# Performance work log

Measured on AMD Instinct MI355X. Metric: run time of the kernel, lower is better.

Reference implementation:

```python
import jax, jax.numpy as jnp
import numpy as np

B, N, H, IN, D, ET = 16, 128, 256, 4, 2, 2
E = N * (N - 1)
NRF = 4 * D + 1            # num_relative_features = 9 (2D)
NODE_F = IN + NRF + D      # 15
EDGE_F = 2 * NRF + IN + D  # 24
EPS = 1e-8


def _norm(v):
    return jnp.sqrt(jnp.sum(v * v, axis=-1, keepdims=True) + EPS)


def _rot(R, v):
    return jnp.einsum('...ij,...j->...i', R, v)


def _relfeat(dp, dv, R, dth):
    # rotation-invariant relative features in frame R: rotated rel pos/vel,
    # distances, polar angles, heading difference -> 2+2+1+1+1+1+1 = 9 dims
    rp = _rot(R, dp)
    rv = _rot(R, dv)
    ang = jnp.arctan2(rp[..., 1:2], rp[..., 0:1])
    vang = jnp.arctan2(rv[..., 1:2], rv[..., 0:1])
    return jnp.concatenate([rp, rv, _norm(dp), ang, _norm(dv), vang, dth], -1)


def _forward(inputs, hidden, edges, predicted_field,
             msg_fc1_w, msg_fc1_b, msg_fc2_w, msg_fc2_b,
             pm_fc1_w, pm_fc1_b, pm_fc2_w, pm_fc2_b,
             hidden_r_w, hidden_i_w, hidden_h_w,
             present_r_w, present_r_b, present_i_w, present_i_b,
             present_n_w, present_n_b,
             input_r_w, input_r_b, input_i_w, input_i_b, input_n_w, input_n_b,
             out_w1, out_b1, out_w2, out_b2, out_w3, out_b3,
             send, recv):
    # ---- recurrent message passing on hidden state ----
    pre_msg = jnp.concatenate([hidden[:, recv], hidden[:, send]], -1)  # [B,E,2H]
    all_msgs = jnp.zeros((B, E, H), pre_msg.dtype)
    for i in range(1, ET):  # skip_first_edge_type = True
        m = jnp.tanh(pre_msg @ msg_fc1_w[i].T + msg_fc1_b[i])
        m = jnp.tanh(m @ msg_fc2_w[i].T + msg_fc2_b[i])
        all_msgs = all_msgs + m * edges[:, :, i:i + 1]
    agg_msgs = jnp.zeros((B, N, H), all_msgs.dtype).at[:, recv].add(all_msgs) / (N - 1)

    # ---- localizer: per-node frame from velocity heading ----
    ext = jnp.concatenate([inputs, predicted_field], -1)  # [B,N,6]
    pos, vel, field = ext[..., :D], ext[..., D:2 * D], ext[..., 2 * D:]
    theta = jnp.arctan2(vel[..., 1], vel[..., 0])  # [B,N]
    c, s = jnp.cos(theta), jnp.sin(theta)
    R = jnp.stack([jnp.stack([c, s], -1), jnp.stack([-s, c], -1)], -2)  # [B,N,2,2]
    Rinv = jnp.swapaxes(R, -1, -2)

    loc_pos, loc_vel, loc_field = _rot(R, pos), _rot(R, vel), _rot(R, field)
    rel_self = _relfeat(pos, vel, R, theta[..., None])
    rel_feat = jnp.concatenate([rel_self, loc_pos, loc_vel, loc_field], -1)  # [B,N,15]

    dp = pos[:, send] - pos[:, recv]
    dv = vel[:, send] - vel[:, recv]
    dth = (theta[:, send] - theta[:, recv])[..., None]
    f1 = _relfeat(dp, dv, R[:, recv], dth)
    f2 = _relfeat(-dp, -dv, R[:, send], -dth)
    edge_attr = jnp.concatenate(
        [f1, f2, loc_pos[:, recv], loc_vel[:, recv], loc_field[:, recv]], -1)  # [B,E,24]

    # ---- present (observation) message passing ----
    present_msgs = jnp.zeros((B, E, H), edge_attr.dtype)
    for i in range(1, ET):
        m = jax.nn.relu(edge_attr @ pm_fc1_w[i].T + pm_fc1_b[i])
        m = jax.nn.relu(m @ pm_fc2_w[i].T + pm_fc2_b[i])
        present_msgs = present_msgs + m * edges[:, :, i:i + 1]
    present_agg = jnp.zeros((B, N, H), present_msgs.dtype).at[:, recv].add(present_msgs) / (N - 1)

    # ---- GRU-style gated update ----
    inp_r = rel_feat @ input_r_w.T + input_r_b + present_agg @ present_r_w.T + present_r_b
    inp_i = rel_feat @ input_i_w.T + input_i_b + present_agg @ present_i_w.T + present_i_b
    inp_n = rel_feat @ input_n_w.T + input_n_b + present_agg @ present_n_w.T + present_n_b
    r = jax.nn.sigmoid(inp_r + agg_msgs @ hidden_r_w.T)
    i_g = jax.nn.sigmoid(inp_i + agg_msgs @ hidden_i_w.T)
    n_g = jnp.tanh(inp_n + r * (agg_msgs @ hidden_h_w.T))
    hidden_new = (1.0 - i_g) * n_g + i_g * hidden

    # ---- output MLP + globalizer ----
    h1 = jax.nn.relu(hidden_new @ out_w1.T + out_b1)
    h2 = jax.nn.relu(h1 @ out_w2.T + out_b2)
    pred = h2 @ out_w3.T + out_b3  # [B,N,4]
    pred_global = jnp.concatenate(
        [_rot(Rinv, pred[..., :D]), _rot(Rinv, pred[..., D:2 * D])], -1)
    outputs = inputs + pred_global
    return outputs, hidden_new


def setup_inputs():
    key = jax.random.key(0)
    ks = iter(jax.random.split(key, 48))
    rn = lambda *s: jax.random.normal(next(ks), s, jnp.float32)
    w = lambda *s: rn(*s) * 0.05
    send, recv = np.where(~np.eye(N, dtype=bool))
    return dict(
        inputs=rn(B, N, IN), hidden=rn(B, N, H),
        edges=jax.random.uniform(next(ks), (B, E, ET), jnp.float32),
        predicted_field=rn(B, N, D),
        msg_fc1_w=w(ET, H, 2 * H), msg_fc1_b=w(ET, H),
        msg_fc2_w=w(ET, H, H), msg_fc2_b=w(ET, H),
        pm_fc1_w=w(ET, H, EDGE_F), pm_fc1_b=w(ET, H),
        pm_fc2_w=w(ET, H, H), pm_fc2_b=w(ET, H),
        hidden_r_w=w(H, H), hidden_i_w=w(H, H), hidden_h_w=w(H, H),
        present_r_w=w(H, H), present_r_b=w(H),
        present_i_w=w(H, H), present_i_b=w(H),
        present_n_w=w(H, H), present_n_b=w(H),
        input_r_w=w(H, NODE_F), input_r_b=w(H),
        input_i_w=w(H, NODE_F), input_i_b=w(H),
        input_n_w=w(H, NODE_F), input_n_b=w(H),
        out_w1=w(H, H), out_b1=w(H), out_w2=w(H, H), out_b2=w(H),
        out_w3=w(IN, H), out_b3=w(IN),
        send_edges=jnp.asarray(send, jnp.int32),
        recv_edges=jnp.asarray(recv, jnp.int32),
    )


def reference(inputs, hidden, edges, predicted_field,
              msg_fc1_w, msg_fc1_b, msg_fc2_w, msg_fc2_b,
              pm_fc1_w, pm_fc1_b, pm_fc2_w, pm_fc2_b,
              hidden_r_w, hidden_i_w, hidden_h_w,
              present_r_w, present_r_b, present_i_w, present_i_b,
              present_n_w, present_n_b,
              input_r_w, input_r_b, input_i_w, input_i_b, input_n_w, input_n_b,
              out_w1, out_b1, out_w2, out_b2, out_w3, out_b3,
              send_edges, recv_edges):
    return _forward(inputs, hidden, edges, predicted_field,
                    msg_fc1_w, msg_fc1_b, msg_fc2_w, msg_fc2_b,
                    pm_fc1_w, pm_fc1_b, pm_fc2_w, pm_fc2_b,
                    hidden_r_w, hidden_i_w, hidden_h_w,
                    present_r_w, present_r_b, present_i_w, present_i_b,
                    present_n_w, present_n_b,
                    input_r_w, input_r_b, input_i_w, input_i_b, input_n_w, input_n_b,
                    out_w1, out_b1, out_w2, out_b2, out_w3, out_b3,
                    send_edges, recv_edges)
```

## Files before the change

kernel.cpp:

```cpp
#include <hip/hip_runtime.h>
#include <math.h>

#define BB 16
#define NN 128
#define HH 256
#define EE (NN*(NN-1))

typedef unsigned short ushort_t;
typedef unsigned int uint_t;
typedef __attribute__((ext_vector_type(8))) short bf16x8;
typedef __attribute__((ext_vector_type(4))) float f32x4;

__device__ __forceinline__ ushort_t f2b(float f) {
  unsigned u = __builtin_bit_cast(unsigned, f);
  unsigned r = (u + 0x7fffu + ((u >> 16) & 1u)) >> 16;
  return (ushort_t)r;
}
__device__ __forceinline__ float blo(uint_t u) {
  return __builtin_bit_cast(float, u << 16);
}
__device__ __forceinline__ float bhi(uint_t u) {
  return __builtin_bit_cast(float, u & 0xffff0000u);
}

__device__ __forceinline__ float fast_tanh(float x) {
  float xx = fminf(fmaxf(x, -15.f), 15.f);
  float e = __builtin_amdgcn_exp2f(xx * 2.8853900817779268f);
  return (e - 1.f) * __builtin_amdgcn_rcpf(e + 1.f);
}
__device__ __forceinline__ float fast_sigmoid(float x) {
  float xx = fminf(fmaxf(x, -30.f), 30.f);
  float e = __builtin_amdgcn_exp2f(-xx * 1.4426950408889634f);
  return __builtin_amdgcn_rcpf(1.f + e);
}

__global__ __launch_bounds__(256) void k_prep(
    const float* __restrict__ inputs, const float* __restrict__ pfield,
    float* __restrict__ geom, float* __restrict__ relf,
    const float* __restrict__ w2, const float* __restrict__ pw2,
    const float* __restrict__ pw1,
    const float* __restrict__ pr_w, const float* __restrict__ pi_w,
    const float* __restrict__ pn_w, const float* __restrict__ hr_w,
    const float* __restrict__ hi_w, const float* __restrict__ hh_w,
    const float* __restrict__ ow1, const float* __restrict__ ow2,
    const float* __restrict__ w1,
    ushort_t* __restrict__ w2b, ushort_t* __restrict__ pw2b,
    ushort_t* __restrict__ pw1b, uint_t* __restrict__ wpk) {
  __shared__ float ltile[64][65];
  int bid = blockIdx.x;
  int tid = threadIdx.x;

  if (bid < 8) {
    int idx = bid * 256 + tid;
    float px = inputs[idx*4+0], py = inputs[idx*4+1];
    float vx = inputs[idx*4+2], vy = inputs[idx*4+3];
    float fx = pfield[idx*2+0], fy = pfield[idx*2+1];
    float th = atan2f(vy, vx);
    float c = cosf(th), s = sinf(th);
    float lpx =  c*px + s*py, lpy = -s*px + c*py;
    float lvx =  c*vx + s*vy, lvy = -s*vx + c*vy;
    float lfx =  c*fx + s*fy, lfy = -s*fx + c*fy;
    float np_ = sqrtf(px*px + py*py + 1e-8f);
    float nv_ = sqrtf(vx*vx + vy*vy + 1e-8f);
    float ang  = atan2f(lpy, lpx);
    float vang = atan2f(lvy, lvx);
    float* g = geom + idx*16;
    g[0]=px; g[1]=py; g[2]=vx; g[3]=vy; g[4]=th; g[5]=c; g[6]=s;
    g[7]=lpx; g[8]=lpy; g[9]=lvx; g[10]=lvy; g[11]=lfx; g[12]=lfy;
    float* r = relf + idx*16;
    r[0]=lpx; r[1]=lpy; r[2]=lvx; r[3]=lvy; r[4]=np_; r[5]=ang; r[6]=nv_; r[7]=vang; r[8]=th;
    r[9]=lpx; r[10]=lpy; r[11]=lvx; r[12]=lvy; r[13]=lfx; r[14]=lfy;
    return;
  }
  if (bid < 552) {
    int idx = (bid - 8) * 256 + tid;
    if (idx < HH*HH) { w2b[idx] = f2b(w2[HH*HH + idx]); return; }
    idx -= HH*HH;
    if (idx < HH*HH) { pw2b[idx] = f2b(pw2[HH*HH + idx]); return; }
    idx -= HH*HH;
    int col = idx >> 5, kk = idx & 31;
    pw1b[idx] = (kk < 24) ? f2b(pw1[col*24 + kk]) : (ushort_t)0;
    return;
  }
  int tb = bid - 552;
  int m  = tb >> 4;
  int sub = tb & 15;
  int Hbase  = (sub >> 2) * 64;
  int k2base = (sub & 3) * 32;
  const float* src; int sstride, soff;
  if      (m == 0) { src = pr_w; sstride = HH; soff = 0; }
  else if (m == 1) { src = pi_w; sstride = HH; soff = 0; }
  else if (m == 2) { src = pn_w; sstride = HH; soff = 0; }
  else if (m == 3) { src = hr_w; sstride = HH; soff = 0; }
  else if (m == 4) { src = hi_w; sstride = HH; soff = 0; }
  else if (m == 5) { src = hh_w; sstride = HH; soff = 0; }
  else if (m == 6) { src = ow1;  sstride = HH; soff = 0; }
  else if (m == 7) { src = ow2;  sstride = HH; soff = 0; }
  else if (m == 8) { src = w1 + HH*2*HH; sstride = 2*HH; soff = 0; }
  else             { src = w1 + HH*2*HH; sstride = 2*HH; soff = HH; }
  int wv = tid >> 6, lane = tid & 63;
  #pragma unroll 4
  for (int i = 0; i < 16; ++i) {
    int rl = wv*16 + i;
    ltile[rl][lane] = src[(Hbase + rl)*sstride + soff + 2*k2base + lane];
  }
  __syncthreads();
  int h_l = tid & 63, kslot = tid >> 6;
  uint_t* dst = wpk + m*32768;
  #pragma unroll
  for (int e = 0; e < 8; ++e) {
    int kk = kslot*8 + e;
    uint_t lo = f2b(ltile[h_l][2*kk]);
    uint_t hi = f2b(ltile[h_l][2*kk + 1]);
    dst[(k2base + kk)*256 + Hbase + h_l] = lo | (hi << 16);
  }
}

__global__ __launch_bounds__(256) void k_hab(const float* __restrict__ hidden,
                                             const uint_t* __restrict__ wpk,
                                             const float* __restrict__ b1,
                                             float* __restrict__ Ha,
                                             float* __restrict__ Hb) {
  int n = blockIdx.x >> 2, qtr = blockIdx.x & 3;
  int tid = threadIdx.x;
  __shared__ float x[4][HH];
  for (int q = 0; q < 4; ++q) {
    int b = qtr*4 + q;
    x[q][tid] = hidden[(b*NN + n)*HH + tid];
  }
  __syncthreads();
  const uint_t* pA = wpk + 8*32768;
  const uint_t* pB = wpk + 9*32768;
  float accA[4], accB[4];
  float bias = b1[HH + tid];
  #pragma unroll
  for (int q = 0; q < 4; ++q) { accA[q] = bias; accB[q] = 0.f; }
  for (int k2 = 0; k2 < 128; ++k2) {
    uint_t ua = pA[(k2<<8) + tid];
    uint_t ub = pB[(k2<<8) + tid];
    float wa0 = blo(ua), wa1 = bhi(ua);
    float wb0 = blo(ub), wb1 = bhi(ub);
    int k = k2 << 1;
    #pragma unroll
    for (int q = 0; q < 4; ++q) {
      float2 x2 = *(const float2*)(&x[q][k]);
      accA[q] += x2.x*wa0 + x2.y*wa1;
      accB[q] += x2.x*wb0 + x2.y*wb1;
    }
  }
  for (int q = 0; q < 4; ++q) {
    int b = qtr*4 + q;
    Ha[(b*NN + n)*HH + tid] = accA[q];
    Hb[(b*NN + n)*HH + tid] = accB[q];
  }
}

__global__ __launch_bounds__(256, 4) void k_edge(
    const float* __restrict__ Ha, const float* __restrict__ Hb,
    const float* __restrict__ geom, const float* __restrict__ edges,
    const ushort_t* __restrict__ w2b, const float* __restrict__ b2,
    const ushort_t* __restrict__ pw2b, const float* __restrict__ pb2,
    const ushort_t* __restrict__ pw1b, const float* __restrict__ pb1,
    float* __restrict__ agg0, float* __restrict__ agg1,
    float* __restrict__ pagg0, float* __restrict__ pagg1) {
  int half = blockIdx.x & 1;
  int j = (blockIdx.x >> 1) & 127;
  int b = blockIdx.x >> 8;
  int tid = threadIdx.x;
  int lane = tid & 63;
  int wv = tid >> 6;
  int lrow = lane & 15, lk = lane >> 4;

  __shared__ __align__(16) unsigned char m1s[64*512];
  __shared__ __align__(16) unsigned char attrB[64*64];
  __shared__ __align__(16) float HajS[HH];
  __shared__ float wgtS[64];
  __shared__ float gjS[13];

  HajS[tid] = Ha[(b*NN + j)*HH + tid];
  if (tid < 13) gjS[tid] = geom[(b*NN + j)*16 + tid];
  __syncthreads();

  if (tid < 64) {
    int il = tid;
    int i = half*64 + il;
    const float* gi = geom + (b*NN + i)*16;
    float dpx = gi[0]-gjS[0], dpy = gi[1]-gjS[1];
    float dvx = gi[2]-gjS[2], dvy = gi[3]-gjS[3];
    float dth = gi[4]-gjS[4];
    float cj = gjS[5], sj = gjS[6];
    float ci = gi[5],  si = gi[6];
    float ndp = sqrtf(dpx*dpx + dpy*dpy + 1e-8f);
    float ndv = sqrtf(dvx*dvx + dvy*dvy + 1e-8f);
    float r1x =  cj*dpx + sj*dpy, r1y = -sj*dpx + cj*dpy;
    float v1x =  cj*dvx + sj*dvy, v1y = -sj*dvx + cj*dvy;
    float r2x = -(ci*dpx + si*dpy), r2y = si*dpx - ci*dpy;
    float v2x = -(ci*dvx + si*dvy), v2y = si*dvx - ci*dvy;
    float f[24];
    f[0]=r1x; f[1]=r1y; f[2]=v1x; f[3]=v1y;
    f[4]=ndp; f[5]=atan2f(r1y, r1x);
    f[6]=ndv; f[7]=atan2f(v1y, v1x); f[8]=dth;
    f[9]=r2x; f[10]=r2y; f[11]=v2x; f[12]=v2y;
    f[13]=ndp; f[14]=atan2f(r2y, r2x);
    f[15]=ndv; f[16]=atan2f(v2y, v2x); f[17]=-dth;
    f[18]=gjS[7]; f[19]=gjS[8]; f[20]=gjS[9];
    f[21]=gjS[10]; f[22]=gjS[11]; f[23]=gjS[12];
    #pragma unroll
    for (int kb = 0; kb < 4; ++kb) {
      bf16x8 v;
      #pragma unroll
      for (int e = 0; e < 8; ++e) {
        int k = kb*8 + e;
        v[e] = (k < 24) ? (short)f2b(f[k]) : (short)0;
      }
      *reinterpret_cast<bf16x8*>(attrB + il*64 + ((kb*16) ^ ((il&3)<<4))) = v;
    }
    float w = 0.f;
    if (i != j) {
      int e = i*127 + (j < i ? j : j-1);
      w = edges[(b*EE + e)*2 + 1];
    }
    wgtS[il] = w;
  }
  __syncthreads();

  {
    int hp = tid & 127;
    int rh = tid >> 7;
    float2 ha2 = *(const float2*)(HajS + 2*hp);
    const float* hbbase = Hb + (b*NN + half*64 + rh*32)*HH + 2*hp;
    #pragma unroll
    for (int r0 = 0; r0 < 32; r0 += 8) {
      float2 v[8];
      #pragma unroll
      for (int u = 0; u < 8; ++u)
        v[u] = *(const float2*)(hbbase + (r0+u)*HH);
      #pragma unroll
      for (int u = 0; u < 8; ++u) {
        int row = rh*32 + r0 + u;
        uint_t lo = f2b(fast_tanh(ha2.x + v[u].x));
        uint_t hi = f2b(fast_tanh(ha2.y + v[u].y));
        *(uint_t*)(m1s + row*512 + ((hp*4) ^ ((row&15)<<4))) = lo | (hi << 16);
      }
    }
  }
  __syncthreads();

  float wreg[16];
  #pragma unroll
  for (int rt = 0; rt < 4; ++rt)
    #pragma unroll
    for (int r = 0; r < 4; ++r)
      wreg[rt*4+r] = wgtS[rt*16 + lk*4 + r];

  {
    f32x4 acc[4][4];
    {
      float bias0 = b2[wv*64 + 0*16 + lrow];
      float bias1 = b2[wv*64 + 1*16 + lrow];
      float bias2 = b2[wv*64 + 2*16 + lrow];
      float bias3 = b2[wv*64 + 3*16 + lrow];
      #pragma unroll
      for (int rt = 0; rt < 4; ++rt) {
        acc[rt][0] = (f32x4){bias0,bias0,bias0,bias0};
        acc[rt][1] = (f32x4){bias1,bias1,bias1,bias1};
        acc[rt][2] = (f32x4){bias2,bias2,bias2,bias2};
        acc[rt][3] = (f32x4){bias3,bias3,bias3,bias3};
      }
    }
    for (int kk = 0; kk < 8; ++kk) {
      bf16x8 afr[4];
      #pragma unroll
      for (int rt = 0; rt < 4; ++rt) {
        int row = rt*16 + lrow;
        afr[rt] = *reinterpret_cast<const bf16x8*>(
            m1s + row*512 + ((kk*64 + lk*16) ^ ((row&15)<<4)));
      }
      #pragma unroll
      for (int nt = 0; nt < 4; ++nt) {
        int col = wv*64 + nt*16 + lrow;
        bf16x8 bfr = *reinterpret_cast<const bf16x8*>(w2b + col*HH + kk*32 + lk*8);
        #pragma unroll
        for (int rt = 0; rt < 4; ++rt)
          acc[rt][nt] = __builtin_amdgcn_mfma_f32_16x16x32_bf16(afr[rt], bfr, acc[rt][nt], 0, 0, 0);
      }
    }
    float* aggOut = half ? agg1 : agg0;
    #pragma unroll
    for (int nt = 0; nt < 4; ++nt) {
      float p = 0.f;
      #pragma unroll
      for (int rt = 0; rt < 4; ++rt)
        #pragma unroll
        for (int r = 0; r < 4; ++r)
          p += fast_tanh(acc[rt][nt][r]) * wreg[rt*4+r];
      p += __shfl_xor(p, 16);
      p += __shfl_xor(p, 32);
      if (lane < 16)
        aggOut[(b*NN + j)*HH + wv*64 + nt*16 + lane] = p * (1.0f/127.0f);
    }
  }
  __syncthreads();

  {
    f32x4 acc[4][4];
    {
      float bias0 = pb1[wv*64 + 0*16 + lrow];
      float bias1 = pb1[wv*64 + 1*16 + lrow];
      float bias2 = pb1[wv*64 + 2*16 + lrow];
      float bias3 = pb1[wv*64 + 3*16 + lrow];
      #pragma unroll
      for (int rt = 0; rt < 4; ++rt) {
        acc[rt][0] = (f32x4){bias0,bias0,bias0,bias0};
        acc[rt][1] = (f32x4){bias1,bias1,bias1,bias1};
        acc[rt][2] = (f32x4){bias2,bias2,bias2,bias2};
        acc[rt][3] = (f32x4){bias3,bias3,bias3,bias3};
      }
    }
    bf16x8 afr[4];
    #pragma unroll
    for (int rt = 0; rt < 4; ++rt) {
      int row = rt*16 + lrow;
      afr[rt] = *reinterpret_cast<const bf16x8*>(
          attrB + row*64 + ((lk*16) ^ ((lrow&3)<<4)));
    }
    #pragma unroll
    for (int nt = 0; nt < 4; ++nt) {
      int col = wv*64 + nt*16 + lrow;
      bf16x8 bfr = *reinterpret_cast<const bf16x8*>(pw1b + col*32 + lk*8);
      #pragma unroll
      for (int rt = 0; rt < 4; ++rt)
        acc[rt][nt] = __builtin_amdgcn_mfma_f32_16x16x32_bf16(afr[rt], bfr, acc[rt][nt], 0, 0, 0);
    }
    #pragma unroll
    for (int nt = 0; nt < 4; ++nt) {
      int col = wv*64 + nt*16 + lrow;
      #pragma unroll
      for (int rt = 0; rt < 4; ++rt)
        #pragma unroll
        for (int r = 0; r < 4; ++r) {
          int row = rt*16 + lk*4 + r;
          *(ushort_t*)(m1s + row*512 + ((col*2) ^ ((row&15)<<4))) =
              f2b(fmaxf(acc[rt][nt][r], 0.f));
        }
    }
  }
  __syncthreads();

  {
    f32x4 acc[4][4];
    {
      float bias0 = pb2[wv*64 + 0*16 + lrow];
      float bias1 = pb2[wv*64 + 1*16 + lrow];
      float bias2 = pb2[wv*64 + 2*16 + lrow];
      float bias3 = pb2[wv*64 + 3*16 + lrow];
      #pragma unroll
      for (int rt = 0; rt < 4; ++rt) {
        acc[rt][0] = (f32x4){bias0,bias0,bias0,bias0};
        acc[rt][1] = (f32x4){bias1,bias1,bias1,bias1};
        acc[rt][2] = (f32x4){bias2,bias2,bias2,bias2};
        acc[rt][3] = (f32x4){bias3,bias3,bias3,bias3};
      }
    }
    for (int kk = 0; kk < 8; ++kk) {
      bf16x8 afr[4];
      #pragma unroll
      for (int rt = 0; rt < 4; ++rt) {
        int row = rt*16 + lrow;
        afr[rt] = *reinterpret_cast<const bf16x8*>(
            m1s + row*512 + ((kk*64 + lk*16) ^ ((row&15)<<4)));
      }
      #pragma unroll
      for (int nt = 0; nt < 4; ++nt) {
        int col = wv*64 + nt*16 + lrow;
        bf16x8 bfr = *reinterpret_cast<const bf16x8*>(pw2b + col*HH + kk*32 + lk*8);
        #pragma unroll
        for (int rt = 0; rt < 4; ++rt)
          acc[rt][nt] = __builtin_amdgcn_mfma_f32_16x16x32_bf16(afr[rt], bfr, acc[rt][nt], 0, 0, 0);
      }
    }
    float* paggOut = half ? pagg1 : pagg0;
    #pragma unroll
    for (int nt = 0; nt < 4; ++nt) {
      float p = 0.f;
      #pragma unroll
      for (int rt = 0; rt < 4; ++rt)
        #pragma unroll
        for (int r = 0; r < 4; ++r)
          p += fmaxf(acc[rt][nt][r], 0.f) * wreg[rt*4+r];
      p += __shfl_xor(p, 16);
      p += __shfl_xor(p, 32);
      if (lane < 16)
        paggOut[(b*NN + j)*HH + wv*64 + nt*16 + lane] = p * (1.0f/127.0f);
    }
  }
}

__global__ __launch_bounds__(256) void k_gru(
    const float* __restrict__ inputs, const float* __restrict__ hidden,
    const float* __restrict__ geom, const float* __restrict__ relf,
    const float* __restrict__ agg0, const float* __restrict__ agg1,
    const float* __restrict__ pagg0, const float* __restrict__ pagg1,
    const uint_t* __restrict__ wpk,
    const float* __restrict__ pr_b, const float* __restrict__ pi_b,
    const float* __restrict__ pn_b,
    const float* __restrict__ ir_w, const float* __restrict__ ir_b,
    const float* __restrict__ ii_w, const float* __restrict__ ii_b,
    const float* __restrict__ in_w, const float* __restrict__ in_b,
    const float* __restrict__ ob1, const float* __restrict__ ob2,
    const float* __restrict__ ow3, const float* __restrict__ ob3,
    float* __restrict__ out_o, float* __restrict__ out_h) {
  int n = blockIdx.x >> 2, qtr = blockIdx.x & 3;
  int tid = threadIdx.x;
  __shared__ float paS[4][HH], agS[4][HH], hS[4][HH], t0S[4][HH], t1S[4][HH];
  __shared__ float relS[4][16];
  __shared__ float predS[4][4];

  for (int q = 0; q < 4; ++q) {
    int b = qtr*4 + q;
    int base = (b*NN + n)*HH;
    paS[q][tid] = pagg0[base + tid] + pagg1[base + tid];
    agS[q][tid] = agg0[base + tid] + agg1[base + tid];
    hS[q][tid]  = hidden[base + tid];
  }
  if (tid < 64) {
    int q = tid >> 4, k = tid & 15;
    int b = qtr*4 + q;
    relS[q][k] = (k < 15) ? relf[(b*NN + n)*16 + k] : 0.f;
  }
  __syncthreads();

  int h = tid;
  const uint_t* pPr = wpk;
  const uint_t* pPi = wpk + 32768;
  const uint_t* pPn = wpk + 2*32768;
  const uint_t* pHr = wpk + 3*32768;
  const uint_t* pHi = wpk + 4*32768;
  const uint_t* pHh = wpk + 5*32768;
  const uint_t* pO1 = wpk + 6*32768;
  const uint_t* pO2 = wpk + 7*32768;

  float aR[4], aI[4], aN[4], aH[4];
  float br = ir_b[h] + pr_b[h];
  float bi = ii_b[h] + pi_b[h];
  float bn = in_b[h] + pn_b[h];
  #pragma unroll
  for (int q = 0; q < 4; ++q) { aR[q]=br; aI[q]=bi; aN[q]=bn; aH[q]=0.f; }

  for (int k = 0; k < 15; ++k) {
    float wr = ir_w[h*15+k], wi = ii_w[h*15+k], wn = in_w[h*15+k];
    #pragma unroll
    for (int q = 0; q < 4; ++q) {
      float x = relS[q][k];
      aR[q] += x*wr; aI[q] += x*wi; aN[q] += x*wn;
    }
  }

  for (int k2 = 0; k2 < 128; ++k2) {
    uint_t upr = pPr[(k2<<8) + h];
    uint_t upi = pPi[(k2<<8) + h];
    uint_t upn = pPn[(k2<<8) + h];
    uint_t uhr = pHr[(k2<<8) + h];
    uint_t uhi = pHi[(k2<<8) + h];
    uint_t uhh = pHh[(k2<<8) + h];
    float pr0 = blo(upr), pr1 = bhi(upr);
    float pi0 = blo(upi), pi1 = bhi(upi);
    float pn0 = blo(upn), pn1 = bhi(upn);
    float hr0 = blo(uhr), hr1 = bhi(uhr);
    float hi0 = blo(uhi), hi1 = bhi(uhi);
    float hh0 = blo(uhh), hh1 = bhi(uhh);
    int k = k2 << 1;
    #pragma unroll
    for (int q = 0; q < 4; ++q) {
      float2 xp = *(const float2*)(&paS[q][k]);
      float2 xa = *(const float2*)(&agS[q][k]);
      aR[q] += xp.x*pr0 + xp.y*pr1 + xa.x*hr0 + xa.y*hr1;
      aI[q] += xp.x*pi0 + xp.y*pi1 + xa.x*hi0 + xa.y*hi1;
      aN[q] += xp.x*pn0 + xp.y*pn1;
      aH[q] += xa.x*hh0 + xa.y*hh1;
    }
  }

  #pragma unroll
  for (int q = 0; q < 4; ++q) {
    int b = qtr*4 + q;
    float r  = fast_sigmoid(aR[q]);
    float ig = fast_sigmoid(aI[q]);
    float ng = fast_tanh(aN[q] + r*aH[q]);
    float hn = (1.f - ig)*ng + ig*hS[q][h];
    out_h[(b*NN + n)*HH + h] = hn;
    t0S[q][h] = hn;
  }
  __syncthreads();

  {
    float a1[4];
    float bias = ob1[h];
    #pragma unroll
    for (int q = 0; q < 4; ++q) a1[q] = bias;
    for (int k2 = 0; k2 < 128; ++k2) {
      uint_t u = pO1[(k2<<8) + h];
      float w0 = blo(u), w1 = bhi(u);
      int k = k2 << 1;
      #pragma unroll
      for (int q = 0; q < 4; ++q) {
        float2 x2 = *(const float2*)(&t0S[q][k]);
        a1[q] += x2.x*w0 + x2.y*w1;
      }
    }
    __syncthreads();
    #pragma unroll
    for (int q = 0; q < 4; ++q) t1S[q][h] = fmaxf(a1[q], 0.f);
  }
  __syncthreads();

  {
    float a2[4];
    float bias = ob2[h];
    #pragma unroll
    for (int q = 0; q < 4; ++q) a2[q] = bias;
    for (int k2 = 0; k2 < 128; ++k2) {
      uint_t u = pO2[(k2<<8) + h];
      float w0 = blo(u), w1 = bhi(u);
      int k = k2 << 1;
      #pragma unroll
      for (int q = 0; q < 4; ++q) {
        float2 x2 = *(const float2*)(&t1S[q][k]);
        a2[q] += x2.x*w0 + x2.y*w1;
      }
    }
    __syncthreads();
    #pragma unroll
    for (int q = 0; q < 4; ++q) t0S[q][h] = fmaxf(a2[q], 0.f);
  }
  __syncthreads();

  if (tid < 16) {
    int o = tid >> 2, q = tid & 3;
    float acc = ob3[o];
    for (int k = 0; k < HH; ++k) acc += t0S[q][k]*ow3[o*HH + k];
    predS[q][o] = acc;
  }
  __syncthreads();
  if (tid < 4) {
    int q = tid;
    int b = qtr*4 + q;
    const float* g = geom + (b*NN + n)*16;
    float c = g[5], s = g[6];
    float p0 = predS[q][0], p1 = predS[q][1], p2 = predS[q][2], p3 = predS[q][3];
    int base = (b*NN + n)*4;
    out_o[base+0] = inputs[base+0] + (c*p0 - s*p1);
    out_o[base+1] = inputs[base+1] + (s*p0 + c*p1);
    out_o[base+2] = inputs[base+2] + (c*p2 - s*p3);
    out_o[base+3] = inputs[base+3] + (s*p2 + c*p3);
  }
}

extern "C" void kernel_launch(void* const* d_in, const int* in_sizes, int n_in,
                              void* d_out, int out_size, void* d_ws, size_t ws_size,
                              hipStream_t stream) {
  const float* inputs    = (const float*)d_in[0];
  const float* hidden    = (const float*)d_in[1];
  const float* edges     = (const float*)d_in[2];
  const float* pfield    = (const float*)d_in[3];
  const float* msg_fc1_w = (const float*)d_in[4];
  const float* msg_fc1_b = (const float*)d_in[5];
  const float* msg_fc2_w = (const float*)d_in[6];
  const float* msg_fc2_b = (const float*)d_in[7];
  const float* pm_fc1_w  = (const float*)d_in[8];
  const float* pm_fc1_b  = (const float*)d_in[9];
  const float* pm_fc2_w  = (const float*)d_in[10];
  const float* pm_fc2_b  = (const float*)d_in[11];
  const float* hr_w = (const float*)d_in[12];
  const float* hi_w = (const float*)d_in[13];
  const float* hh_w = (const float*)d_in[14];
  const float* pr_w = (const float*)d_in[15];
  const float* pr_b = (const float*)d_in[16];
  const float* pi_w = (const float*)d_in[17];
  const float* pi_b = (const float*)d_in[18];
  const float* pn_w = (const float*)d_in[19];
  const float* pn_b = (const float*)d_in[20];
  const float* ir_w = (const float*)d_in[21];
  const float* ir_b = (const float*)d_in[22];
  const float* ii_w = (const float*)d_in[23];
  const float* ii_b = (const float*)d_in[24];
  const float* in_w = (const float*)d_in[25];
  const float* in_b = (const float*)d_in[26];
  const float* ow1  = (const float*)d_in[27];
  const float* ob1  = (const float*)d_in[28];
  const float* ow2  = (const float*)d_in[29];
  const float* ob2  = (const float*)d_in[30];
  const float* ow3  = (const float*)d_in[31];
  const float* ob3  = (const float*)d_in[32];

  float* ws   = (float*)d_ws;
  float* geom = ws;
  float* relf = geom + 32768;
  float* Ha   = relf + 32768;
  float* Hb   = Ha   + 524288;
  float* agg0 = Hb   + 524288;
  float* agg1 = agg0 + 524288;
  float* pagg0= agg1 + 524288;
  float* pagg1= pagg0+ 524288;
  ushort_t* w2b  = (ushort_t*)(pagg1 + 524288);
  ushort_t* pw2b = w2b + HH*HH;
  ushort_t* pw1b = pw2b + HH*HH;
  uint_t*   wpk  = (uint_t*)(pw1b + HH*32);

  float* out_o = (float*)d_out;
  float* out_h = out_o + BB*NN*4;

  k_prep<<<dim3(712), dim3(256), 0, stream>>>(inputs, pfield, geom, relf,
      msg_fc2_w, pm_fc2_w, pm_fc1_w + HH*24,
      pr_w, pi_w, pn_w, hr_w, hi_w, hh_w, ow1, ow2,
      msg_fc1_w, w2b, pw2b, pw1b, wpk);
  k_hab<<<dim3(512), dim3(256), 0, stream>>>(hidden, wpk, msg_fc1_b, Ha, Hb);
  k_edge<<<dim3(BB*NN*2), dim3(256), 0, stream>>>(Ha, Hb, geom, edges,
      w2b, msg_fc2_b + HH, pw2b, pm_fc2_b + HH,
      pw1b, pm_fc1_b + HH, agg0, agg1, pagg0, pagg1);
  k_gru<<<dim3(512), dim3(256), 0, stream>>>(inputs, hidden, geom, relf,
      agg0, agg1, pagg0, pagg1, wpk,
      pr_b, pi_b, pn_b, ir_w, ir_b, ii_w, ii_b, in_w, in_b,
      ob1, ob2, ow3, ob3, out_o, out_h);
}
```

Measured before the change: 411.6 us.

## Split edge kernel into quarter-row tiles with four partial aggregation buffers

Each edge block now handles 32 sender rows instead of 64, doubling the grid to 8192 blocks and halving shared memory and accumulator registers. Launch bounds are raised to target 8 blocks per CU, and the per-quarter partial sums go to four strided buffers that the GRU kernel adds together. One __syncthreads is removed by reading Ha directly from global memory instead of staging it in shared memory. In exchange, each block reuses every streamed weight fragment across half as many rows, so weight traffic per edge doubles, and the extra partial buffers add write and read traffic.

```diff
diff --git a/kernel.cpp b/kernel.cpp
--- a/kernel.cpp
+++ b/kernel.cpp
@@ -5,6 +5,7 @@
 #define NN 128
 #define HH 256
 #define EE (NN*(NN-1))
+#define AGSTRIDE 524288
 
 typedef unsigned short ushort_t;
 typedef unsigned int uint_t;
@@ -155,35 +156,32 @@
   }
 }
 
-__global__ __launch_bounds__(256, 4) void k_edge(
+__global__ __launch_bounds__(256, 8) void k_edge(
     const float* __restrict__ Ha, const float* __restrict__ Hb,
     const float* __restrict__ geom, const float* __restrict__ edges,
     const ushort_t* __restrict__ w2b, const float* __restrict__ b2,
     const ushort_t* __restrict__ pw2b, const float* __restrict__ pb2,
     const ushort_t* __restrict__ pw1b, const float* __restrict__ pb1,
-    float* __restrict__ agg0, float* __restrict__ agg1,
-    float* __restrict__ pagg0, float* __restrict__ pagg1) {
-  int half = blockIdx.x & 1;
-  int j = (blockIdx.x >> 1) & 127;
-  int b = blockIdx.x >> 8;
+    float* __restrict__ agg, float* __restrict__ pagg) {
+  int qt = blockIdx.x & 3;
+  int j = (blockIdx.x >> 2) & 127;
+  int b = blockIdx.x >> 9;
   int tid = threadIdx.x;
   int lane = tid & 63;
   int wv = tid >> 6;
   int lrow = lane & 15, lk = lane >> 4;
 
-  __shared__ __align__(16) unsigned char m1s[64*512];
-  __shared__ __align__(16) unsigned char attrB[64*64];
-  __shared__ __align__(16) float HajS[HH];
-  __shared__ float wgtS[64];
+  __shared__ __align__(16) unsigned char m1s[32*512];
+  __shared__ __align__(16) unsigned char attrB[32*64];
+  __shared__ float wgtS[32];
   __shared__ float gjS[13];
 
-  HajS[tid] = Ha[(b*NN + j)*HH + tid];
   if (tid < 13) gjS[tid] = geom[(b*NN + j)*16 + tid];
   __syncthreads();
 
-  if (tid < 64) {
+  if (tid < 32) {
     int il = tid;
-    int i = half*64 + il;
+    int i = qt*32 + il;
     const float* gi = geom + (b*NN + i)*16;
     float dpx = gi[0]-gjS[0], dpy = gi[1]-gjS[1];
     float dvx = gi[2]-gjS[2], dvy = gi[3]-gjS[3];
@@ -222,22 +220,22 @@
     }
     wgtS[il] = w;
   }
-  __syncthreads();
 
   {
     int hp = tid & 127;
     int rh = tid >> 7;
-    float2 ha2 = *(const float2*)(HajS + 2*hp);
-    const float* hbbase = Hb + (b*NN + half*64 + rh*32)*HH + 2*hp;
-    #pragma unroll
-    for (int r0 = 0; r0 < 32; r0 += 8) {
-      float2 v[8];
-      #pragma unroll
-      for (int u = 0; u < 8; ++u)
+    const float* haptr = Ha + (b*NN + j)*HH + 2*hp;
+    float2 ha2 = { haptr[0], haptr[1] };
+    const float* hbbase = Hb + (b*NN + qt*32 + rh*16)*HH + 2*hp;
+    #pragma unroll
+    for (int r0 = 0; r0 < 16; r0 += 4) {
+      float2 v[4];
+      #pragma unroll
+      for (int u = 0; u < 4; ++u)
         v[u] = *(const float2*)(hbbase + (r0+u)*HH);
       #pragma unroll
-      for (int u = 0; u < 8; ++u) {
-        int row = rh*32 + r0 + u;
+      for (int u = 0; u < 4; ++u) {
+        int row = rh*16 + r0 + u;
         uint_t lo = f2b(fast_tanh(ha2.x + v[u].x));
         uint_t hi = f2b(fast_tanh(ha2.y + v[u].y));
         *(uint_t*)(m1s + row*512 + ((hp*4) ^ ((row&15)<<4))) = lo | (hi << 16);
@@ -246,32 +244,25 @@
   }
   __syncthreads();
 
-  float wreg[16];
+  float wreg[8];
   #pragma unroll
-  for (int rt = 0; rt < 4; ++rt)
+  for (int rt = 0; rt < 2; ++rt)
     #pragma unroll
     for (int r = 0; r < 4; ++r)
       wreg[rt*4+r] = wgtS[rt*16 + lk*4 + r];
 
   {
-    f32x4 acc[4][4];
-    {
-      float bias0 = b2[wv*64 + 0*16 + lrow];
-      float bias1 = b2[wv*64 + 1*16 + lrow];
-      float bias2 = b2[wv*64 + 2*16 + lrow];
-      float bias3 = b2[wv*64 + 3*16 + lrow];
-      #pragma unroll
-      for (int rt = 0; rt < 4; ++rt) {
-        acc[rt][0] = (f32x4){bias0,bias0,bias0,bias0};
-        acc[rt][1] = (f32x4){bias1,bias1,bias1,bias1};
-        acc[rt][2] = (f32x4){bias2,bias2,bias2,bias2};
-        acc[rt][3] = (f32x4){bias3,bias3,bias3,bias3};
-      }
+    f32x4 acc[2][4];
+    #pragma unroll
+    for (int nt = 0; nt < 4; ++nt) {
+      float bias = b2[wv*64 + nt*16 + lrow];
+      acc[0][nt] = (f32x4){bias,bias,bias,bias};
+      acc[1][nt] = (f32x4){bias,bias,bias,bias};
     }
     for (int kk = 0; kk < 8; ++kk) {
-      bf16x8 afr[4];
-      #pragma unroll
-      for (int rt = 0; rt < 4; ++rt) {
+      bf16x8 afr[2];
+      #pragma unroll
+      for (int rt = 0; rt < 2; ++rt) {
         int row = rt*16 + lrow;
         afr[rt] = *reinterpret_cast<const bf16x8*>(
             m1s + row*512 + ((kk*64 + lk*16) ^ ((row&15)<<4)));
@@ -281,16 +272,16 @@
         int col = wv*64 + nt*16 + lrow;
         bf16x8 bfr = *reinterpret_cast<const bf16x8*>(w2b + col*HH + kk*32 + lk*8);
         #pragma unroll
-        for (int rt = 0; rt < 4; ++rt)
+        for (int rt = 0; rt < 2; ++rt)
           acc[rt][nt] = __builtin_amdgcn_mfma_f32_16x16x32_bf16(afr[rt], bfr, acc[rt][nt], 0, 0, 0);
       }
     }
-    float* aggOut = half ? agg1 : agg0;
+    float* aggOut = agg + qt*AGSTRIDE;
     #pragma unroll
     for (int nt = 0; nt < 4; ++nt) {
       float p = 0.f;
       #pragma unroll
-      for (int rt = 0; rt < 4; ++rt)
+      for (int rt = 0; rt < 2; ++rt)
         #pragma unroll
         for (int r = 0; r < 4; ++r)
           p += fast_tanh(acc[rt][nt][r]) * wreg[rt*4+r];
@@ -303,23 +294,16 @@
   __syncthreads();
 
   {
-    f32x4 acc[4][4];
-    {
-      float bias0 = pb1[wv*64 + 0*16 + lrow];
-      float bias1 = pb1[wv*64 + 1*16 + lrow];
-      float bias2 = pb1[wv*64 + 2*16 + lrow];
-      float bias3 = pb1[wv*64 + 3*16 + lrow];
-      #pragma unroll
-      for (int rt = 0; rt < 4; ++rt) {
-        acc[rt][0] = (f32x4){bias0,bias0,bias0,bias0};
-        acc[rt][1] = (f32x4){bias1,bias1,bias1,bias1};
-        acc[rt][2] = (f32x4){bias2,bias2,bias2,bias2};
-        acc[rt][3] = (f32x4){bias3,bias3,bias3,bias3};
-      }
-    }
-    bf16x8 afr[4];
-    #pragma unroll
-    for (int rt = 0; rt < 4; ++rt) {
+    f32x4 acc[2][4];
+    #pragma unroll
+    for (int nt = 0; nt < 4; ++nt) {
+      float bias = pb1[wv*64 + nt*16 + lrow];
+      acc[0][nt] = (f32x4){bias,bias,bias,bias};
+      acc[1][nt] = (f32x4){bias,bias,bias,bias};
+    }
+    bf16x8 afr[2];
+    #pragma unroll
+    for (int rt = 0; rt < 2; ++rt) {
       int row = rt*16 + lrow;
       afr[rt] = *reinterpret_cast<const bf16x8*>(
           attrB + row*64 + ((lk*16) ^ ((lrow&3)<<4)));
@@ -329,14 +313,14 @@
       int col = wv*64 + nt*16 + lrow;
       bf16x8 bfr = *reinterpret_cast<const bf16x8*>(pw1b + col*32 + lk*8);
       #pragma unroll
-      for (int rt = 0; rt < 4; ++rt)
+      for (int rt = 0; rt < 2; ++rt)
         acc[rt][nt] = __builtin_amdgcn_mfma_f32_16x16x32_bf16(afr[rt], bfr, acc[rt][nt], 0, 0, 0);
     }
     #pragma unroll
     for (int nt = 0; nt < 4; ++nt) {
       int col = wv*64 + nt*16 + lrow;
       #pragma unroll
-      for (int rt = 0; rt < 4; ++rt)
+      for (int rt = 0; rt < 2; ++rt)
         #pragma unroll
         for (int r = 0; r < 4; ++r) {
           int row = rt*16 + lk*4 + r;
@@ -348,24 +332,17 @@
   __syncthreads();
 
   {
-    f32x4 acc[4][4];
-    {
-      float bias0 = pb2[wv*64 + 0*16 + lrow];
-      float bias1 = pb2[wv*64 + 1*16 + lrow];
-      float bias2 = pb2[wv*64 + 2*16 + lrow];
-      float bias3 = pb2[wv*64 + 3*16 + lrow];
-      #pragma unroll
-      for (int rt = 0; rt < 4; ++rt) {
-        acc[rt][0] = (f32x4){bias0,bias0,bias0,bias0};
-        acc[rt][1] = (f32x4){bias1,bias1,bias1,bias1};
-        acc[rt][2] = (f32x4){bias2,bias2,bias2,bias2};
-        acc[rt][3] = (f32x4){bias3,bias3,bias3,bias3};
-      }
+    f32x4 acc[2][4];
+    #pragma unroll
+    for (int nt = 0; nt < 4; ++nt) {
+      float bias = pb2[wv*64 + nt*16 + lrow];
+      acc[0][nt] = (f32x4){bias,bias,bias,bias};
+      acc[1][nt] = (f32x4){bias,bias,bias,bias};
     }
     for (int kk = 0; kk < 8; ++kk) {
-      bf16x8 afr[4];
-      #pragma unroll
-      for (int rt = 0; rt < 4; ++rt) {
+      bf16x8 afr[2];
+      #pragma unroll
+      for (int rt = 0; rt < 2; ++rt) {
         int row = rt*16 + lrow;
         afr[rt] = *reinterpret_cast<const bf16x8*>(
             m1s + row*512 + ((kk*64 + lk*16) ^ ((row&15)<<4)));
@@ -375,16 +352,16 @@
         int col = wv*64 + nt*16 + lrow;
         bf16x8 bfr = *reinterpret_cast<const bf16x8*>(pw2b + col*HH + kk*32 + lk*8);
         #pragma unroll
-        for (int rt = 0; rt < 4; ++rt)
+        for (int rt = 0; rt < 2; ++rt)
           acc[rt][nt] = __builtin_amdgcn_mfma_f32_16x16x32_bf16(afr[rt], bfr, acc[rt][nt], 0, 0, 0);
       }
     }
-    float* paggOut = half ? pagg1 : pagg0;
+    float* paggOut = pagg + qt*AGSTRIDE;
     #pragma unroll
     for (int nt = 0; nt < 4; ++nt) {
       float p = 0.f;
       #pragma unroll
-      for (int rt = 0; rt < 4; ++rt)
+      for (int rt = 0; rt < 2; ++rt)
         #pragma unroll
         for (int r = 0; r < 4; ++r)
           p += fmaxf(acc[rt][nt][r], 0.f) * wreg[rt*4+r];
@@ -399,8 +376,7 @@
 __global__ __launch_bounds__(256) void k_gru(
     const float* __restrict__ inputs, const float* __restrict__ hidden,
     const float* __restrict__ geom, const float* __restrict__ relf,
-    const float* __restrict__ agg0, const float* __restrict__ agg1,
-    const float* __restrict__ pagg0, const float* __restrict__ pagg1,
+    const float* __restrict__ agg, const float* __restrict__ pagg,
     const uint_t* __restrict__ wpk,
     const float* __restrict__ pr_b, const float* __restrict__ pi_b,
     const float* __restrict__ pn_b,
@@ -418,10 +394,12 @@
 
   for (int q = 0; q < 4; ++q) {
     int b = qtr*4 + q;
-    int base = (b*NN + n)*HH;
-    paS[q][tid] = pagg0[base + tid] + pagg1[base + tid];
-    agS[q][tid] = agg0[base + tid] + agg1[base + tid];
-    hS[q][tid]  = hidden[base + tid];
+    int base = (b*NN + n)*HH + tid;
+    paS[q][tid] = pagg[base] + pagg[AGSTRIDE + base] +
+                  pagg[2*AGSTRIDE + base] + pagg[3*AGSTRIDE + base];
+    agS[q][tid] = agg[base] + agg[AGSTRIDE + base] +
+                  agg[2*AGSTRIDE + base] + agg[3*AGSTRIDE + base];
+    hS[q][tid]  = hidden[base];
   }
   if (tid < 64) {
     int q = tid >> 4, k = tid & 15;
@@ -598,11 +576,9 @@
   float* relf = geom + 32768;
   float* Ha   = relf + 32768;
   float* Hb   = Ha   + 524288;
-  float* agg0 = Hb   + 524288;
-  float* agg1 = agg0 + 524288;
-  float* pagg0= agg1 + 524288;
-  float* pagg1= pagg0+ 524288;
-  ushort_t* w2b  = (ushort_t*)(pagg1 + 524288);
+  float* agg  = Hb   + 524288;
+  float* pagg = agg  + 4*AGSTRIDE;
+  ushort_t* w2b  = (ushort_t*)(pagg + 4*AGSTRIDE);
   ushort_t* pw2b = w2b + HH*HH;
   ushort_t* pw1b = pw2b + HH*HH;
   uint_t*   wpk  = (uint_t*)(pw1b + HH*32);
@@ -615,11 +591,11 @@
       pr_w, pi_w, pn_w, hr_w, hi_w, hh_w, ow1, ow2,
       msg_fc1_w, w2b, pw2b, pw1b, wpk);
   k_hab<<<dim3(512), dim3(256), 0, stream>>>(hidden, wpk, msg_fc1_b, Ha, Hb);
-  k_edge<<<dim3(BB*NN*2), dim3(256), 0, stream>>>(Ha, Hb, geom, edges,
+  k_edge<<<dim3(BB*NN*4), dim3(256), 0, stream>>>(Ha, Hb, geom, edges,
       w2b, msg_fc2_b + HH, pw2b, pm_fc2_b + HH,
-      pw1b, pm_fc1_b + HH, agg0, agg1, pagg0, pagg1);
+      pw1b, pm_fc1_b + HH, agg, pagg);
   k_gru<<<dim3(512), dim3(256), 0, stream>>>(inputs, hidden, geom, relf,
-      agg0, agg1, pagg0, pagg1, wpk,
+      agg, pagg, wpk,
       pr_b, pi_b, pn_b, ir_w, ir_b, ii_w, ii_b, in_w, in_b,
       ob1, ob2, ow3, ob3, out_o, out_h);
 }
```

After: 627.4 us. +52.5%, slower.
